# Kernel tuning notes

Measured on AMD Instinct MI355X. Metric: run time of the kernel, lower is better.

The kernel has to match this reference:

```python
import jax, jax.numpy as jnp
import numpy as np

DIM = 128
N_HEADS = 4
HEAD_DIM = DIM // N_HEADS  # 32
RANK = 8
SCALING = 16.0 / RANK      # alpha / rank = 2.0
ROPE_BASE = 10000.0
INV_SQRT_HD = 1.0 / float(np.sqrt(HEAD_DIM))


def _rope(x, cos, sin):
    # x: [B, S, H, D]; interleaved-pair rotation matching torch view(..., -1, 2)
    B, S, H, D = x.shape
    xr = x.reshape(B, S, H, D // 2, 2)
    x1, x2 = xr[..., 0], xr[..., 1]
    c = cos[None, :, None, :]  # [1, S, 1, D/2]
    s = sin[None, :, None, :]
    out = jnp.stack([x1 * c - x2 * s, x1 * s + x2 * c], axis=-1)
    return out.reshape(B, S, H, D)


def setup_inputs() -> dict:
    key = jax.random.key(0)
    ks = jax.random.split(key, 11)
    B, S = 128, 256
    w = lambda k, shp: jax.random.normal(k, shp, dtype=jnp.float32) * 0.05
    return {
        "x": jax.random.normal(ks[0], (B, S, DIM), dtype=jnp.float32),
        "wq": w(ks[1], (DIM, DIM)),
        "wk": w(ks[2], (DIM, DIM)),
        "wv": w(ks[3], (DIM, DIM)),
        "wo": w(ks[4], (DIM, DIM)),
        "lora_A_q": w(ks[5], (RANK, DIM)),
        "lora_B_q": w(ks[6], (DIM, RANK)),
        "lora_A_k": w(ks[7], (RANK, DIM)),
        "lora_B_k": w(ks[8], (DIM, RANK)),
        "lora_A_v": w(ks[9], (RANK, DIM)),
        "lora_B_v": w(ks[10], (DIM, RANK)),
    }


def reference(x, wq, wk, wv, wo, lora_A_q, lora_B_q, lora_A_k, lora_B_k,
              lora_A_v, lora_B_v):
    B, S, _ = x.shape
    # RoPE tables (HEAD_DIM split into pairs)
    pos = jnp.arange(S, dtype=jnp.float32)
    inv_freq = 1.0 / (ROPE_BASE ** (jnp.arange(0, HEAD_DIM, 2, dtype=jnp.float32) / HEAD_DIM))
    freqs = pos[:, None] * inv_freq[None, :]  # [S, HEAD_DIM/2]
    cos, sin = jnp.cos(freqs), jnp.sin(freqs)

    def proj(w, A, Bm):
        # base linear (no bias) + LoRA low-rank delta (dropout = eval identity)
        return x @ w.T + (x @ A.T @ Bm.T) * SCALING

    q = proj(wq, lora_A_q, lora_B_q).reshape(B, S, N_HEADS, HEAD_DIM)
    k = proj(wk, lora_A_k, lora_B_k).reshape(B, S, N_HEADS, HEAD_DIM)
    v = proj(wv, lora_A_v, lora_B_v).reshape(B, S, N_HEADS, HEAD_DIM)

    q = _rope(q, cos, sin).transpose(0, 2, 1, 3)  # [B, H, S, D]
    k = _rope(k, cos, sin).transpose(0, 2, 1, 3)
    v = v.transpose(0, 2, 1, 3)

    scores = jnp.einsum('bhqd,bhkd->bhqk', q, k) * INV_SQRT_HD
    causal = jnp.triu(jnp.ones((S, S), dtype=bool), k=1)
    scores = jnp.where(causal[None, None], -jnp.inf, scores)
    attn = jax.nn.softmax(scores, axis=-1)

    out = jnp.einsum('bhqk,bhkd->bhqd', attn, v)
    out = out.transpose(0, 2, 1, 3).reshape(B, S, DIM)
    return out @ wo.T
```

## Files before the change

### kernel.cpp

```cpp
#include <hip/hip_runtime.h>
#include <math.h>

typedef __attribute__((ext_vector_type(8))) short short8;
typedef __attribute__((ext_vector_type(4))) float floatx4;

#define NH 4
#define HD 32
#define DIM 128
#define SEQ 256
#define BATCH 128
#define BS (BATCH*SEQ)
#define RANK 8
#define SCALING 2.0f
#define INV_SQRT_HD 0.17677669529663687f

#define QB_OFF  (0ull)
#define KB_OFF  (8ull<<20)
#define VT_OFF  (16ull<<20)
#define XB_OFF  (24ull<<20)
#define WE_OFF  (32ull<<20)
#define TAB_OFF (33ull<<20)

static __device__ __forceinline__ unsigned short f2bf(float f) {
    unsigned u = __float_as_uint(f);
    unsigned r = (u + 0x7FFFu + ((u >> 16) & 1u)) >> 16;
    return (unsigned short)r;
}
static __device__ __forceinline__ unsigned packbf(float lo, float hi) {
    return (unsigned)f2bf(lo) | ((unsigned)f2bf(hi) << 16);
}

__global__ __launch_bounds__(256) void prep_kernel(
    const float* __restrict__ x,
    const float* __restrict__ wq, const float* __restrict__ wk,
    const float* __restrict__ wv, const float* __restrict__ wo,
    const float* __restrict__ Aq, const float* __restrict__ Bq,
    const float* __restrict__ Ak, const float* __restrict__ Bk,
    const float* __restrict__ Av, const float* __restrict__ Bv,
    unsigned short* __restrict__ weffL, float* __restrict__ tab,
    unsigned short* __restrict__ xbL)
{
    const int bid = blockIdx.x, tid = threadIdx.x;
    if (bid < 32) {
        int t = bid * 256 + tid;
        int m    = t >> 11;
        int kc   = (t >> 9) & 3;
        int s    = (t >> 6) & 7;
        int lane = t & 63;
        int m16 = lane & 15, quad = lane >> 4;
        int row = (m < 3) ? ((s >> 1) * 32 + 2 * m16 + (s & 1)) : (s * 16 + m16);
        int col0 = kc * 32 + quad * 8;
        const float* W = m == 0 ? wq : (m == 1 ? wk : (m == 2 ? wv : wo));
        const float* A  = m == 0 ? Aq : (m == 1 ? Ak : Av);
        const float* Bm = m == 0 ? Bq : (m == 1 ? Bk : Bv);
        union { uint4 u4; unsigned short us[8]; } frag;
#pragma unroll
        for (int j = 0; j < 8; j++) {
            float val = W[row * DIM + col0 + j];
            if (m < 3) {
                float sacc = 0.f;
#pragma unroll
                for (int r = 0; r < RANK; r++)
                    sacc += Bm[row * RANK + r] * A[r * DIM + col0 + j];
                val += SCALING * sacc;
            }
            if (m == 0) val *= INV_SQRT_HD;
            frag.us[j] = f2bf(val);
        }
        *(uint4*)(weffL + (size_t)t * 8) = frag.u4;
    } else if (bid < 48) {
        int gid = (bid - 32) * 256 + tid;
        int spos = gid >> 4, i = gid & 15;
        float invf = exp2f(-0.83048202f * (float)i);
        float ang = (float)spos * invf;
        float c, s;
        sincosf(ang, &s, &c);
        tab[gid * 2]     = c;
        tab[gid * 2 + 1] = s;
    } else {
        int t = (bid - 48) * 256 + tid;
        int g    = t >> 8;
        int kc   = (t >> 6) & 3;
        int lane = t & 63;
        int m16 = lane & 15, quad = lane >> 4;
        const float* xp = x + (size_t)(g * 16 + m16) * DIM + kc * 32 + quad * 8;
        float4 f0 = *(const float4*)xp;
        float4 f1 = *(const float4*)(xp + 4);
        uint4 o;
        o.x = packbf(f0.x, f0.y); o.y = packbf(f0.z, f0.w);
        o.z = packbf(f1.x, f1.y); o.w = packbf(f1.z, f1.w);
        *(uint4*)(xbL + (size_t)t * 8) = o;
    }
}

#define VSU_STRIDE 66
__global__ __launch_bounds__(256) void qkv_kernel(
    const unsigned short* __restrict__ xbL, const unsigned short* __restrict__ weffL,
    const float* __restrict__ tab,
    unsigned* __restrict__ qb, unsigned* __restrict__ kb,
    unsigned short* __restrict__ vtL)
{
    __shared__ unsigned vs_u[64 * VSU_STRIDE];

    const int which = blockIdx.y;
    const unsigned short* W = weffL + which * DIM * DIM;

    const int tid = threadIdx.x;
    const int w = __builtin_amdgcn_readfirstlane(tid >> 6);
    const int lane = tid & 63;
    const int m16 = lane & 15, quad = lane >> 4;
    const int g = blockIdx.x * 4 + w;
    const int b = g >> 4;

    short8 afrag[4];
#pragma unroll
    for (int kc = 0; kc < 4; kc++)
        afrag[kc] = *(const short8*)(xbL + ((size_t)(g * 4 + kc) * 64 + lane) * 8);

    floatx4 acc_e[NH], acc_o[NH];
#pragma unroll
    for (int h = 0; h < NH; h++) {
        acc_e[h] = (floatx4){0.f, 0.f, 0.f, 0.f};
        acc_o[h] = (floatx4){0.f, 0.f, 0.f, 0.f};
    }

#pragma unroll
    for (int kc = 0; kc < 4; kc++) {
#pragma unroll
        for (int h = 0; h < NH; h++) {
            const unsigned short* base = W + ((kc * 8 + h * 2) * 64 + lane) * 8;
            short8 be = *(const short8*)base;
            short8 bo = *(const short8*)(base + 512);
            acc_e[h] = __builtin_amdgcn_mfma_f32_16x16x32_bf16(afrag[kc], be, acc_e[h], 0, 0, 0);
            acc_o[h] = __builtin_amdgcn_mfma_f32_16x16x32_bf16(afrag[kc], bo, acc_o[h], 0, 0, 0);
        }
    }

    if (which < 2) {
        unsigned* outp = which == 0 ? qb : kb;
        const int sposq = (g & 15) * 16 + quad * 4;
#pragma unroll
        for (int r = 0; r < 4; r++) {
            int spos = sposq + r;
            float2 cs = *(const float2*)(tab + ((size_t)spos * 16 + m16) * 2);
#pragma unroll
            for (int h = 0; h < NH; h++) {
                float e = acc_e[h][r], o = acc_o[h][r];
                outp[((size_t)(b * NH + h) * SEQ + spos) * (HD / 2) + m16] =
                    packbf(e * cs.x - o * cs.y, e * cs.y + o * cs.x);
            }
        }
    } else {
        const int tokb = w * 16 + quad * 4;
#pragma unroll
        for (int r = 0; r < 4; r++)
#pragma unroll
            for (int h = 0; h < NH; h++)
                vs_u[(tokb + r) * VSU_STRIDE + h * 16 + m16] =
                    packbf(acc_e[h][r], acc_o[h][r]);
        __syncthreads();
        const unsigned short* vs_s = (const unsigned short*)vs_u;
        const int cb = ((blockIdx.x * 64) & 255) >> 5;
#pragma unroll
        for (int it = 0; it < 4; it++) {
            int f = it * 256 + tid;
            int c_l = f >> 9;
            int h   = (f >> 7) & 3;
            int p   = (f >> 6) & 1;
            int ln  = f & 63;
            int fm16 = ln & 15, fq = ln >> 4;
            unsigned short tmp[8];
#pragma unroll
            for (int j = 0; j < 8; j++)
                tmp[j] = vs_s[(c_l * 32 + fq * 8 + j) * (VSU_STRIDE * 2) + h * 32 + 2 * fm16 + p];
            uint4 o;
            o.x = (unsigned)tmp[0] | ((unsigned)tmp[1] << 16);
            o.y = (unsigned)tmp[2] | ((unsigned)tmp[3] << 16);
            o.z = (unsigned)tmp[4] | ((unsigned)tmp[5] << 16);
            o.w = (unsigned)tmp[6] | ((unsigned)tmp[7] << 16);
            size_t bh = (size_t)(b * NH + h);
            *(uint4*)(vtL + ((bh * 8 + cb + c_l) * 2 + p) * 512 + ln * 8) = o;
        }
    }
}

#define PB_STRIDE 40
#define OS_STRIDE 136
__global__ __launch_bounds__(256) void attn_kernel(
    const unsigned short* __restrict__ qbs, const unsigned short* __restrict__ kbs,
    const unsigned short* __restrict__ vtL, const unsigned short* __restrict__ woL,
    float* __restrict__ out)
{
    __shared__ unsigned short pbuf[4][2][16 * PB_STRIDE];
    __shared__ unsigned short os[32 * OS_STRIDE];

    const int qt = blockIdx.x;
    const int b  = blockIdx.y;
    const int q0 = qt * 32;
    const int tid = threadIdx.x;
    const int w = __builtin_amdgcn_readfirstlane(tid >> 6);
    const int lane = tid & 63;
    const int m16 = lane & 15, quad = lane >> 4;

    const size_t bh = (size_t)(b * NH + w);
    const unsigned short* qrow = qbs + (bh * SEQ + q0) * HD;
    const unsigned short* krow = kbs + bh * SEQ * HD;
    const unsigned short* vbase = vtL + bh * 8 * 1024;

    short8 aq[2];
#pragma unroll
    for (int qs = 0; qs < 2; qs++)
        aq[qs] = *(const short8*)(qrow + (size_t)(qs * 16 + m16) * HD + quad * 8);

    const short ob = (short)0x3F80;
    const short8 bones = {ob, ob, ob, ob, ob, ob, ob, ob};

    floatx4 o_e[2], o_o[2], o_l[2];
#pragma unroll
    for (int qs = 0; qs < 2; qs++) {
        o_e[qs] = (floatx4){0.f, 0.f, 0.f, 0.f};
        o_o[qs] = (floatx4){0.f, 0.f, 0.f, 0.f};
        o_l[qs] = (floatx4){0.f, 0.f, 0.f, 0.f};
    }

    const floatx4 z4 = (floatx4){0.f, 0.f, 0.f, 0.f};
    const int nchunks = qt + 1;

    short8 cbk0, cbk1, cbve, cbvo, nbk0, nbk1, nbve, nbvo;
    {
        const unsigned short* kp = krow;
        cbk0 = *(const short8*)(kp + (size_t)m16 * HD + quad * 8);
        cbk1 = *(const short8*)(kp + (size_t)(16 + m16) * HD + quad * 8);
        const unsigned short* vp = vbase + lane * 8;
        cbve = *(const short8*)vp;
        cbvo = *(const short8*)(vp + 512);
    }

    for (int c = 0; c < nchunks; c++) {
        const int cn = (c + 1 < nchunks) ? c + 1 : c;
        {
            const unsigned short* kp = krow + (size_t)cn * 32 * HD;
            nbk0 = *(const short8*)(kp + (size_t)m16 * HD + quad * 8);
            nbk1 = *(const short8*)(kp + (size_t)(16 + m16) * HD + quad * 8);
            const unsigned short* vp = vbase + (size_t)cn * 1024 + lane * 8;
            nbve = *(const short8*)vp;
            nbvo = *(const short8*)(vp + 512);
        }
        const int k0 = c * 32;
#pragma unroll
        for (int qs = 0; qs < 2; qs++) {
            floatx4 s0 = __builtin_amdgcn_mfma_f32_16x16x32_bf16(aq[qs], cbk0, z4, 0, 0, 0);
            floatx4 s1 = __builtin_amdgcn_mfma_f32_16x16x32_bf16(aq[qs], cbk1, z4, 0, 0, 0);
            unsigned short* pw = pbuf[w][qs];
            const int qg = q0 + qs * 16 + quad * 4;
#pragma unroll
            for (int t = 0; t < 2; t++) {
                int kg = k0 + t * 16 + m16;
#pragma unroll
                for (int r = 0; r < 4; r++) {
                    float sc = t ? s1[r] : s0[r];
                    float p = (kg <= qg + r) ? __expf(sc) : 0.f;
                    pw[(quad * 4 + r) * PB_STRIDE + t * 16 + m16] = f2bf(p);
                }
            }
            short8 ap = *(const short8*)(pw + m16 * PB_STRIDE + quad * 8);
            o_e[qs] = __builtin_amdgcn_mfma_f32_16x16x32_bf16(ap, cbve, o_e[qs], 0, 0, 0);
            o_o[qs] = __builtin_amdgcn_mfma_f32_16x16x32_bf16(ap, cbvo, o_o[qs], 0, 0, 0);
            o_l[qs] = __builtin_amdgcn_mfma_f32_16x16x32_bf16(ap, bones, o_l[qs], 0, 0, 0);
        }
        cbk0 = nbk0; cbk1 = nbk1; cbve = nbve; cbvo = nbvo;
    }

    unsigned* osu = (unsigned*)os;
#pragma unroll
    for (int qs = 0; qs < 2; qs++)
#pragma unroll
        for (int r = 0; r < 4; r++) {
            float inv = 1.f / o_l[qs][r];
            osu[(qs * 16 + quad * 4 + r) * (OS_STRIDE / 2) + w * 16 + m16] =
                packbf(o_e[qs][r] * inv, o_o[qs][r] * inv);
        }
    __syncthreads();

    const int tw = (w & 1) * 16;
    const int dbase = (w >> 1) * 64;

    short8 af[4];
#pragma unroll
    for (int kc = 0; kc < 4; kc++)
        af[kc] = *(const short8*)(os + (tw + m16) * OS_STRIDE + kc * 32 + quad * 8);

    floatx4 acc[4];
#pragma unroll
    for (int nt = 0; nt < 4; nt++) acc[nt] = (floatx4){0.f, 0.f, 0.f, 0.f};
#pragma unroll
    for (int kc = 0; kc < 4; kc++)
#pragma unroll
        for (int nt = 0; nt < 4; nt++) {
            short8 bf = *(const short8*)(woL + ((kc * 8 + (w >> 1) * 4 + nt) * 64 + lane) * 8);
            acc[nt] = __builtin_amdgcn_mfma_f32_16x16x32_bf16(af[kc], bf, acc[nt], 0, 0, 0);
        }

#pragma unroll
    for (int nt = 0; nt < 4; nt++)
#pragma unroll
        for (int r = 0; r < 4; r++)
            out[(size_t)(b * SEQ + q0 + tw + quad * 4 + r) * DIM
                + dbase + nt * 16 + m16] = acc[nt][r];
}

extern "C" void kernel_launch(void* const* d_in, const int* in_sizes, int n_in,
                              void* d_out, int out_size, void* d_ws, size_t ws_size,
                              hipStream_t stream)
{
    const float* x  = (const float*)d_in[0];
    const float* wq = (const float*)d_in[1];
    const float* wk = (const float*)d_in[2];
    const float* wv = (const float*)d_in[3];
    const float* wo = (const float*)d_in[4];
    const float* Aq = (const float*)d_in[5];
    const float* Bq = (const float*)d_in[6];
    const float* Ak = (const float*)d_in[7];
    const float* Bk = (const float*)d_in[8];
    const float* Av = (const float*)d_in[9];
    const float* Bv = (const float*)d_in[10];
    float* out = (float*)d_out;
    char* ws = (char*)d_ws;

    unsigned*       qb    = (unsigned*)(ws + QB_OFF);
    unsigned*       kb    = (unsigned*)(ws + KB_OFF);
    unsigned short* vtL   = (unsigned short*)(ws + VT_OFF);
    unsigned short* xbL   = (unsigned short*)(ws + XB_OFF);
    unsigned short* weffL = (unsigned short*)(ws + WE_OFF);
    float*          tab   = (float*)(ws + TAB_OFF);

    prep_kernel<<<48 + 2048, 256, 0, stream>>>(
        x, wq, wk, wv, wo, Aq, Bq, Ak, Bk, Av, Bv, weffL, tab, xbL);
    qkv_kernel<<<dim3(BS / 64, 3), 256, 0, stream>>>(xbL, weffL, tab, qb, kb, vtL);
    attn_kernel<<<dim3(8, BATCH), 256, 0, stream>>>(
        (const unsigned short*)qb, (const unsigned short*)kb, vtL,
        weffL + 3 * DIM * DIM, out);
}
```

Before: 127.4 us.

## Interleave key order in V layout, pack P with perm, use exp2

Folds log2(e) into the Q weight scaling so the softmax can call the hardware exp2 instead of __expf. P values for two key tiles are packed into one 32-bit LDS write with a byte-permute bf16 pack. To match that order, the V transpose in the QKV kernel now stores keys interleaved. It also uses a swizzled LDS layout so the transpose reads are vectorized uint4 loads instead of scalar short gathers. The key ordering now couples the two kernels and must stay consistent between them.

```diff
diff --git a/kernel.cpp b/kernel.cpp
--- a/kernel.cpp
+++ b/kernel.cpp
@@ -13,6 +13,13 @@
 #define RANK 8
 #define SCALING 2.0f
 #define INV_SQRT_HD 0.17677669529663687f
+#define LOG2E 1.4426950408889634f
+
+#if __has_builtin(__builtin_amdgcn_exp2f)
+#define EXP2F __builtin_amdgcn_exp2f
+#else
+#define EXP2F exp2f
+#endif
 
 #define QB_OFF  (0ull)
 #define KB_OFF  (8ull<<20)
@@ -23,11 +30,13 @@
 
 static __device__ __forceinline__ unsigned short f2bf(float f) {
     unsigned u = __float_as_uint(f);
-    unsigned r = (u + 0x7FFFu + ((u >> 16) & 1u)) >> 16;
-    return (unsigned short)r;
+    return (unsigned short)((u + 0x7FFFu + ((u >> 16) & 1u)) >> 16);
 }
 static __device__ __forceinline__ unsigned packbf(float lo, float hi) {
-    return (unsigned)f2bf(lo) | ((unsigned)f2bf(hi) << 16);
+    unsigned ua = __float_as_uint(lo), ub = __float_as_uint(hi);
+    ua += 0x7FFFu + ((ua >> 16) & 1u);
+    ub += 0x7FFFu + ((ub >> 16) & 1u);
+    return __builtin_amdgcn_perm(ub, ua, 0x07060302);
 }
 
 __global__ __launch_bounds__(256) void prep_kernel(
@@ -64,7 +73,7 @@
                     sacc += Bm[row * RANK + r] * A[r * DIM + col0 + j];
                 val += SCALING * sacc;
             }
-            if (m == 0) val *= INV_SQRT_HD;
+            if (m == 0) val *= INV_SQRT_HD * LOG2E;
             frag.us[j] = f2bf(val);
         }
         *(uint4*)(weffL + (size_t)t * 8) = frag.u4;
@@ -93,14 +102,14 @@
     }
 }
 
-#define VSU_STRIDE 66
+#define VSTU 68
 __global__ __launch_bounds__(256) void qkv_kernel(
     const unsigned short* __restrict__ xbL, const unsigned short* __restrict__ weffL,
     const float* __restrict__ tab,
     unsigned* __restrict__ qb, unsigned* __restrict__ kb,
     unsigned short* __restrict__ vtL)
 {
-    __shared__ unsigned vs_u[64 * VSU_STRIDE];
+    __shared__ unsigned vs_u[64 * VSTU];
 
     const int which = blockIdx.y;
     const unsigned short* W = weffL + which * DIM * DIM;
@@ -151,16 +160,19 @@
             }
         }
     } else {
-        const int tokb = w * 16 + quad * 4;
-#pragma unroll
-        for (int r = 0; r < 4; r++)
+        const int cloc = w >> 1;
+        const int sig0 = (w & 1);
+#pragma unroll
+        for (int r = 0; r < 4; r++) {
+            int sig = 8 * quad + 2 * r + sig0;
+            int col = cloc * 32 + (sig ^ ((m16 & 3) << 3));
 #pragma unroll
             for (int h = 0; h < NH; h++)
-                vs_u[(tokb + r) * VSU_STRIDE + h * 16 + m16] =
-                    packbf(acc_e[h][r], acc_o[h][r]);
+                vs_u[(h * 16 + m16) * VSTU + col] = packbf(acc_e[h][r], acc_o[h][r]);
+        }
         __syncthreads();
-        const unsigned short* vs_s = (const unsigned short*)vs_u;
         const int cb = ((blockIdx.x * 64) & 255) >> 5;
+        const size_t bhbase = (size_t)(b * NH) * 8;
 #pragma unroll
         for (int it = 0; it < 4; it++) {
             int f = it * 256 + tid;
@@ -169,29 +181,29 @@
             int p   = (f >> 6) & 1;
             int ln  = f & 63;
             int fm16 = ln & 15, fq = ln >> 4;
-            unsigned short tmp[8];
-#pragma unroll
-            for (int j = 0; j < 8; j++)
-                tmp[j] = vs_s[(c_l * 32 + fq * 8 + j) * (VSU_STRIDE * 2) + h * 32 + 2 * fm16 + p];
+            const unsigned* src = vs_u + (h * 16 + fm16) * VSTU + c_l * 32
+                                + ((fq ^ (fm16 & 3)) * 8);
+            uint4 a = *(const uint4*)src;
+            uint4 bb = *(const uint4*)(src + 4);
+            unsigned sel = p ? 0x07060302u : 0x05040100u;
             uint4 o;
-            o.x = (unsigned)tmp[0] | ((unsigned)tmp[1] << 16);
-            o.y = (unsigned)tmp[2] | ((unsigned)tmp[3] << 16);
-            o.z = (unsigned)tmp[4] | ((unsigned)tmp[5] << 16);
-            o.w = (unsigned)tmp[6] | ((unsigned)tmp[7] << 16);
-            size_t bh = (size_t)(b * NH + h);
-            *(uint4*)(vtL + ((bh * 8 + cb + c_l) * 2 + p) * 512 + ln * 8) = o;
-        }
-    }
-}
-
-#define PB_STRIDE 40
+            o.x = __builtin_amdgcn_perm(a.y,  a.x,  sel);
+            o.y = __builtin_amdgcn_perm(a.w,  a.z,  sel);
+            o.z = __builtin_amdgcn_perm(bb.y, bb.x, sel);
+            o.w = __builtin_amdgcn_perm(bb.w, bb.z, sel);
+            *(uint4*)(vtL + (((bhbase + h * 8 + cb + c_l) * 2 + p) * 512 + ln * 8)) = o;
+        }
+    }
+}
+
+#define PBU 20
 #define OS_STRIDE 136
 __global__ __launch_bounds__(256) void attn_kernel(
     const unsigned short* __restrict__ qbs, const unsigned short* __restrict__ kbs,
     const unsigned short* __restrict__ vtL, const unsigned short* __restrict__ woL,
     float* __restrict__ out)
 {
-    __shared__ unsigned short pbuf[4][2][16 * PB_STRIDE];
+    __shared__ unsigned pbuf_u[4 * 2 * 16 * PBU];
     __shared__ unsigned short os[32 * OS_STRIDE];
 
     const int qt = blockIdx.x;
@@ -228,13 +240,14 @@
 
     short8 cbk0, cbk1, cbve, cbvo, nbk0, nbk1, nbve, nbvo;
     {
-        const unsigned short* kp = krow;
-        cbk0 = *(const short8*)(kp + (size_t)m16 * HD + quad * 8);
-        cbk1 = *(const short8*)(kp + (size_t)(16 + m16) * HD + quad * 8);
+        cbk0 = *(const short8*)(krow + (size_t)m16 * HD + quad * 8);
+        cbk1 = *(const short8*)(krow + (size_t)(16 + m16) * HD + quad * 8);
         const unsigned short* vp = vbase + lane * 8;
         cbve = *(const short8*)vp;
         cbvo = *(const short8*)(vp + 512);
     }
+
+    unsigned* pw = pbuf_u + (w * 2) * 16 * PBU;
 
     for (int c = 0; c < nchunks; c++) {
         const int cn = (c + 1 < nchunks) ? c + 1 : c;
@@ -247,23 +260,21 @@
             nbvo = *(const short8*)(vp + 512);
         }
         const int k0 = c * 32;
+        const int kg0 = k0 + m16, kg1 = k0 + 16 + m16;
 #pragma unroll
         for (int qs = 0; qs < 2; qs++) {
             floatx4 s0 = __builtin_amdgcn_mfma_f32_16x16x32_bf16(aq[qs], cbk0, z4, 0, 0, 0);
             floatx4 s1 = __builtin_amdgcn_mfma_f32_16x16x32_bf16(aq[qs], cbk1, z4, 0, 0, 0);
-            unsigned short* pw = pbuf[w][qs];
+            unsigned* pq = pw + qs * 16 * PBU;
             const int qg = q0 + qs * 16 + quad * 4;
 #pragma unroll
-            for (int t = 0; t < 2; t++) {
-                int kg = k0 + t * 16 + m16;
-#pragma unroll
-                for (int r = 0; r < 4; r++) {
-                    float sc = t ? s1[r] : s0[r];
-                    float p = (kg <= qg + r) ? __expf(sc) : 0.f;
-                    pw[(quad * 4 + r) * PB_STRIDE + t * 16 + m16] = f2bf(p);
-                }
+            for (int r = 0; r < 4; r++) {
+                float p0 = (kg0 <= qg + r) ? EXP2F(s0[r]) : 0.f;
+                float p1 = (kg1 <= qg + r) ? EXP2F(s1[r]) : 0.f;
+                pq[(quad * 4 + r) * PBU + m16] = packbf(p0, p1);
             }
-            short8 ap = *(const short8*)(pw + m16 * PB_STRIDE + quad * 8);
+            const unsigned short* pqs = (const unsigned short*)pq;
+            short8 ap = *(const short8*)(pqs + m16 * (PBU * 2) + quad * 8);
             o_e[qs] = __builtin_amdgcn_mfma_f32_16x16x32_bf16(ap, cbve, o_e[qs], 0, 0, 0);
             o_o[qs] = __builtin_amdgcn_mfma_f32_16x16x32_bf16(ap, cbvo, o_o[qs], 0, 0, 0);
             o_l[qs] = __builtin_amdgcn_mfma_f32_16x16x32_bf16(ap, bones, o_l[qs], 0, 0, 0);
```

New measurement: 127.7 us. About the same (+0.2%).
